# Kernel optimization log

Hardware: AMD Instinct MI355X
Metric: run time of the kernel (lower is better)

Reference implementation:

```python
import jax, jax.numpy as jnp
import numpy as np

SIGMA = 1.2
SIGMA_SQ = jnp.float32(SIGMA * SIGMA)


def setup_inputs() -> dict:
    key = jax.random.key(0)
    k1, k2, k3 = jax.random.split(key, 3)
    X = jax.random.normal(k1, (32768, 2), dtype=jnp.float32)
    pattern_layer = jax.random.normal(k2, (8192, 2), dtype=jnp.float32)
    W2 = jax.random.normal(k3, (8192,), dtype=jnp.float32)
    return {"X": X, "pattern_layer": pattern_layer, "W2": W2}


def reference(X, pattern_layer, W2):
    # Pairwise squared distances via |a|^2 + |b|^2 - 2 a.b  -> [N, P]
    x_sq = jnp.sum(X * X, axis=1, keepdims=True)              # [N, 1]
    p_sq = jnp.sum(pattern_layer * pattern_layer, axis=1)     # [P]
    cross = X @ pattern_layer.T                               # [N, P]
    Dsq = x_sq + p_sq[None, :] - 2.0 * cross                  # [N, P]
    K = jnp.exp(-Dsq / (2.0 * SIGMA_SQ))                      # RBF kernel [N, P]
    num = K @ W2                                              # [N]
    den = jnp.sum(K, axis=1)                                  # [N]
    return num / den
```

## Files before the change

### kernel.cpp

```cpp
#include <hip/hip_runtime.h>

#define N 32768
#define P 8192
#define MX 8
#define XG 2
#define PH 2
#define THREADS (XG * PH * 64)
#define XPB (XG * MX)
#define NBLK (N / XPB)
#define PAIRS (P / 2)
#define PAIRS_PER_PH (PAIRS / PH)
#define ITERS (PAIRS_PER_PH / 64)

#define RBF_F 0.50093577808645257f

typedef float v2f __attribute__((ext_vector_type(2)));

static __device__ __forceinline__ float fast_exp2(float x) {
#if __has_builtin(__builtin_amdgcn_exp2f)
    return __builtin_amdgcn_exp2f(x);
#else
    return exp2f(x);
#endif
}

__global__ void prep_kernel(const float* __restrict__ pat,
                            const float* __restrict__ w2,
                            float4* __restrict__ c) {
    int q = blockIdx.x * blockDim.x + threadIdx.x;
    if (q < P / 2) {
        float p00 = pat[4 * q + 0], p01 = pat[4 * q + 1];
        float p10 = pat[4 * q + 2], p11 = pat[4 * q + 3];
        float4 a, b;
        a.x = 2.0f * RBF_F * p00;  a.y = 2.0f * RBF_F * p10;
        a.z = 2.0f * RBF_F * p01;  a.w = 2.0f * RBF_F * p11;
        b.x = -RBF_F * (p00 * p00 + p01 * p01);
        b.y = -RBF_F * (p10 * p10 + p11 * p11);
        b.z = w2[2 * q];           b.w = w2[2 * q + 1];
        c[2 * q]     = a;
        c[2 * q + 1] = b;
    }
}

__global__ __launch_bounds__(THREADS) void
rbf_kernel(const float* __restrict__ X,
           const float4* __restrict__ c,
           float* __restrict__ out) {
    const int t    = threadIdx.x;
    const int lane = t & 63;
    const int w    = __builtin_amdgcn_readfirstlane(t >> 6);
    const int xg   = w >> 1;
    const int ph   = w & 1;

    const int xb = blockIdx.x * XPB + xg * MX;
    const float2* Xp = (const float2*)X;
    v2f xs0[MX], xs1[MX];
#pragma unroll
    for (int i = 0; i < MX; ++i) {
        float2 xv = Xp[xb + i];
        xs0[i] = (v2f){xv.x, xv.x};
        xs1[i] = (v2f){xv.y, xv.y};
    }

    v2f num2[MX], den2[MX];
#pragma unroll
    for (int i = 0; i < MX; ++i) {
        num2[i] = (v2f){0.f, 0.f};
        den2[i] = (v2f){0.f, 0.f};
    }

    const float4* __restrict__ C4 = c + (size_t)ph * (2 * PAIRS_PER_PH);

    float4 a = C4[2 * lane];
    float4 b = C4[2 * lane + 1];

    for (int j = 0; j < ITERS; ++j) {
        const int qn = (((j + 1) & (ITERS - 1)) << 6) + lane;
        float4 an = C4[2 * qn];
        float4 bn = C4[2 * qn + 1];

#pragma unroll
        for (int i = 0; i < MX; ++i) {
            v2f tt = __builtin_elementwise_fma((v2f){a.x, a.y}, xs0[i],
                                               (v2f){b.x, b.y});
            tt = __builtin_elementwise_fma((v2f){a.z, a.w}, xs1[i], tt);
            v2f k = (v2f){fast_exp2(tt.x), fast_exp2(tt.y)};
            den2[i] += k;
            num2[i] = __builtin_elementwise_fma(k, (v2f){b.z, b.w}, num2[i]);
        }
        a = an;
        b = bn;
    }

    float num[MX], den[MX];
#pragma unroll
    for (int i = 0; i < MX; ++i) {
        num[i] = num2[i].x + num2[i].y;
        den[i] = den2[i].x + den2[i].y;
    }
#pragma unroll
    for (int m = 1; m < 64; m <<= 1) {
#pragma unroll
        for (int i = 0; i < MX; ++i) {
            num[i] += __shfl_xor(num[i], m, 64);
            den[i] += __shfl_xor(den[i], m, 64);
        }
    }

    __shared__ float red[XG][PH][MX][2];
    if (lane == 0) {
#pragma unroll
        for (int i = 0; i < MX; ++i) {
            red[xg][ph][i][0] = num[i];
            red[xg][ph][i][1] = den[i];
        }
    }
    __syncthreads();

    if (t < XPB) {
        int g = t >> 3, xi = t & 7;
        float nn = red[g][0][xi][0] + red[g][1][xi][0];
        float dd = red[g][0][xi][1] + red[g][1][xi][1];
        out[blockIdx.x * XPB + t] = nn / dd;
    }
}

extern "C" void kernel_launch(void* const* d_in, const int* in_sizes, int n_in,
                              void* d_out, int out_size, void* d_ws, size_t ws_size,
                              hipStream_t stream) {
    const float* X   = (const float*)d_in[0];
    const float* pat = (const float*)d_in[1];
    const float* w2  = (const float*)d_in[2];
    float* out = (float*)d_out;
    float4* c = (float4*)d_ws;

    prep_kernel<<<(P / 2 + 255) / 256, 256, 0, stream>>>(pat, w2, c);
    rbf_kernel<<<NBLK, THREADS, 0, stream>>>(X, c, out);
}
```

Baseline: 96.48 us.

## Double block size, deepen coefficient prefetch, and stagger start phase per block

Doubles the x-groups per block to 4 (512 threads) and adds a min-blocks-per-CU launch bound. The coefficient stream is prefetched two iterations ahead with the loop unrolled by two. Each block starts at a different rotation of the pattern table, so concurrent blocks read different cache lines. The aim is to hide global load latency better and spread cache traffic, at the cost of register pressure from the extra prefetch buffers, which may clash with the occupancy bound.

```diff
diff --git a/kernel.cpp b/kernel.cpp
--- a/kernel.cpp
+++ b/kernel.cpp
@@ -3,7 +3,7 @@
 #define N 32768
 #define P 8192
 #define MX 8
-#define XG 2
+#define XG 4
 #define PH 2
 #define THREADS (XG * PH * 64)
 #define XPB (XG * MX)
@@ -42,7 +42,19 @@
     }
 }
 
-__global__ __launch_bounds__(THREADS) void
+#define BODY(aa, bb)                                                          \
+    _Pragma("unroll")                                                         \
+    for (int i = 0; i < MX; ++i) {                                            \
+        v2f tt = __builtin_elementwise_fma((v2f){(aa).x, (aa).y}, xs0[i],     \
+                                           (v2f){(bb).x, (bb).y});            \
+        tt = __builtin_elementwise_fma((v2f){(aa).z, (aa).w}, xs1[i], tt);    \
+        v2f k = (v2f){fast_exp2(tt.x), fast_exp2(tt.y)};                      \
+        den2[i] += k;                                                         \
+        num2[i] = __builtin_elementwise_fma(k, (v2f){(bb).z, (bb).w},         \
+                                            num2[i]);                        \
+    }
+
+__global__ __launch_bounds__(THREADS, 4) void
 rbf_kernel(const float* __restrict__ X,
            const float4* __restrict__ c,
            float* __restrict__ out) {
@@ -71,25 +83,22 @@
 
     const float4* __restrict__ C4 = c + (size_t)ph * (2 * PAIRS_PER_PH);
 
-    float4 a = C4[2 * lane];
-    float4 b = C4[2 * lane + 1];
+    const int phase = blockIdx.x & (ITERS - 1);
 
-    for (int j = 0; j < ITERS; ++j) {
-        const int qn = (((j + 1) & (ITERS - 1)) << 6) + lane;
-        float4 an = C4[2 * qn];
-        float4 bn = C4[2 * qn + 1];
+    const int s0 = 2 * (((phase & (ITERS - 1)) << 6) + lane);
+    const int s1 = 2 * ((((phase + 1) & (ITERS - 1)) << 6) + lane);
+    float4 A0 = C4[s0], B0 = C4[s0 + 1];
+    float4 A1 = C4[s1], B1 = C4[s1 + 1];
 
-#pragma unroll
-        for (int i = 0; i < MX; ++i) {
-            v2f tt = __builtin_elementwise_fma((v2f){a.x, a.y}, xs0[i],
-                                               (v2f){b.x, b.y});
-            tt = __builtin_elementwise_fma((v2f){a.z, a.w}, xs1[i], tt);
-            v2f k = (v2f){fast_exp2(tt.x), fast_exp2(tt.y)};
-            den2[i] += k;
-            num2[i] = __builtin_elementwise_fma(k, (v2f){b.z, b.w}, num2[i]);
-        }
-        a = an;
-        b = bn;
+    for (int j = 0; j < ITERS; j += 2) {
+        const int s2 = 2 * ((((phase + j + 2) & (ITERS - 1)) << 6) + lane);
+        float4 an = C4[s2], bn = C4[s2 + 1];
+        BODY(A0, B0)
+        const int s3 = 2 * ((((phase + j + 3) & (ITERS - 1)) << 6) + lane);
+        float4 am = C4[s3], bm = C4[s3 + 1];
+        BODY(A1, B1)
+        A0 = an; B0 = bn;
+        A1 = am; B1 = bm;
     }
 
     float num[MX], den[MX];
```

Measured after the change: 94.29 us (median of 2 runs). 2.3% less time.
